# Optimization experiments

Measured on AMD Instinct MI355X. Metric: run time of the kernel, lower is better.

## Reference

```python
import jax, jax.numpy as jnp
import numpy as np
import math

B, S, D, H = 2, 2048, 2048, 16
DH = D // H
SCALE = math.sqrt(DH)


def setup_inputs() -> dict:
    key = jax.random.key(0)
    ks = jax.random.split(key, 9)
    x = jax.random.normal(ks[0], (B, S, D), dtype=jnp.float32)
    # causal mask: True above the diagonal -> masked (matches masked_fill(mask, -inf))
    mask = jnp.triu(jnp.ones((S, S), dtype=jnp.bool_), k=1)
    std = 0.02
    wq = jax.random.normal(ks[1], (D, D), jnp.float32) * std
    wk = jax.random.normal(ks[2], (D, D), jnp.float32) * std
    wv = jax.random.normal(ks[3], (D, D), jnp.float32) * std
    wo = jax.random.normal(ks[4], (D, D), jnp.float32) * std
    bq = jnp.zeros((D,), jnp.float32)
    bk = jnp.zeros((D,), jnp.float32)
    bv = jnp.zeros((D,), jnp.float32)
    bo = jnp.zeros((D,), jnp.float32)
    return {"x": x, "mask": mask, "wq": wq, "bq": bq, "wk": wk, "bk": bk,
            "wv": wv, "bv": bv, "wo": wo, "bo": bo}


def reference(x, mask, wq, bq, wk, bk, wv, bv, wo, bo):
    b, s, d = x.shape
    # projections (nn.Linear: y = x @ W^T + b)
    q = (x @ wq.T + bq).reshape(b, s, H, DH).transpose(0, 2, 1, 3)  # [b,h,s,dh]
    k = (x @ wk.T + bk).reshape(b, s, H, DH).transpose(0, 2, 1, 3)
    v = (x @ wv.T + bv).reshape(b, s, H, DH).transpose(0, 2, 1, 3)
    scores = jnp.einsum('bhqd,bhkd->bhqk', q, k) / SCALE
    scores = jnp.where(mask[None, None, :, :], -jnp.inf, scores)
    attn = jax.nn.softmax(scores, axis=-1)
    out = jnp.einsum('bhqk,bhkd->bhqd', attn, v)  # [b,h,s,dh]
    out = out.transpose(0, 2, 1, 3).reshape(b, s, d)
    return out @ wo.T + bo
```

## Files before the change

kernel.cpp:

```cpp
#include <hip/hip_runtime.h>
#include <hip/hip_bf16.h>


using u16 = unsigned short;
typedef float  f32x4  __attribute__((ext_vector_type(4)));
typedef short  short8 __attribute__((ext_vector_type(8)));

#define DEV __device__ __forceinline__

constexpr int Bc = 2, Sc = 2048, Dc = 2048, Hc = 16, DHc = 128, Mc = 4096, Kc = 2048;
constexpr float RSCALE = 0.08838834764831845f;
constexpr float L2E    = 1.44269504088896341f;

DEV u16 f2bf(float f) { __bf16 h = (__bf16)f; return __builtin_bit_cast(u16, h); }

DEV void gload_lds16(const void* gsrc, void* lds) {
  __builtin_amdgcn_global_load_lds(
      (const __attribute__((address_space(1))) unsigned int*)gsrc,
      (__attribute__((address_space(3))) unsigned int*)lds, 16, 0, 0);
}

__global__ void cast_all(const float* __restrict__ x, const float* __restrict__ wq,
                         const float* __restrict__ wk, const float* __restrict__ wv,
                         const float* __restrict__ wo, u16* __restrict__ XB,
                         u16* __restrict__ WQKV, u16* __restrict__ WOb) {
  const int i = blockIdx.x * blockDim.x + threadIdx.x;
  const float4* src;
  u16* dst;
  if (i < 2097152)      { src = (const float4*)x  + i;             dst = XB   + (size_t)i * 4; }
  else if (i < 3145728) { src = (const float4*)wq + (i - 2097152); dst = WQKV + (size_t)(i - 2097152) * 4; }
  else if (i < 4194304) { src = (const float4*)wk + (i - 3145728); dst = WQKV + 4194304 + (size_t)(i - 3145728) * 4; }
  else if (i < 5242880) { src = (const float4*)wv + (i - 4194304); dst = WQKV + 8388608 + (size_t)(i - 4194304) * 4; }
  else                  { src = (const float4*)wo + (i - 5242880); dst = WOb  + (size_t)(i - 5242880) * 4; }
  float4 v = *src;
  u16 o0 = f2bf(v.x), o1 = f2bf(v.y), o2 = f2bf(v.z), o3 = f2bf(v.w);
  dst[0] = o0; dst[1] = o1; dst[2] = o2; dst[3] = o3;
}

__global__ __launch_bounds__(512, 2) void gemm8p_qkv(
    const u16* __restrict__ A, const u16* __restrict__ W,
    const float* __restrict__ bq, const float* __restrict__ bk,
    const float* __restrict__ bv,
    u16* __restrict__ q_out, u16* __restrict__ k_out, u16* __restrict__ v_out) {
  __shared__ u16 lsA[2][256 * 64];
  __shared__ u16 lsB[2][256 * 64];
  const int tid = threadIdx.x;
  const int lane = tid & 63;
  const int w = tid >> 6;
  const int wr = w >> 2, wc = w & 3;
  const int l15 = lane & 15, l4 = lane >> 4;

  const int id = blockIdx.x;
  const int wg = (id & 7) * 48 + (id >> 3);
  const int bx = wg >> 4;
  const int by = wg & 15;
  const int m0 = by * 256, n0 = bx * 256;

  constexpr int NT = Kc / 64;

  const int srow = tid >> 3;
  const int spc = tid & 7;
  const int slc = spc ^ (srow & 7);

  auto stA = [&](int buf, int t, int mq, int h) {
    const int r = h * 128 + mq * 64 + srow;
    gload_lds16(A + (size_t)(m0 + r) * Kc + t * 64 + slc * 8,
                &lsA[buf][(h * 128 + mq * 64) * 64 + tid * 8]);
  };
  auto stB = [&](int buf, int t, int nq, int j) {
    const int rr = j * 64 + srow;
    const int n = nq * 32 + (rr >> 5) * 64 + (rr & 31);
    gload_lds16(W + (size_t)(n0 + n) * Kc + t * 64 + slc * 8,
                &lsB[buf][(nq * 128 + j * 64) * 64 + tid * 8]);
  };

  const int pc0 = l4 ^ (l15 & 7);
  const int pc1 = (4 + l4) ^ (l15 & 7);
  const int rA = wr * 128 + l15;
  const int rB = wc * 32 + l15;

  f32x4 acc[8][4] = {};
  short8 af[8], b0[4], b1[4];

  auto ldA = [&](int buf, int mq) {
#pragma unroll
    for (int fm = 0; fm < 4; ++fm) {
      const u16* base = &lsA[buf][(rA + mq * 64 + fm * 16) * 64];
      af[fm * 2 + 0] = *(const short8*)(base + pc0 * 8);
      af[fm * 2 + 1] = *(const short8*)(base + pc1 * 8);
    }
  };
  auto ldB = [&](int buf, int nq, short8* bf) {
#pragma unroll
    for (int fr = 0; fr < 2; ++fr) {
      const u16* base = &lsB[buf][(nq * 128 + rB + fr * 16) * 64];
      bf[fr * 2 + 0] = *(const short8*)(base + pc0 * 8);
      bf[fr * 2 + 1] = *(const short8*)(base + pc1 * 8);
    }
  };
  auto mma = [&](const short8* bf, int mo, int no) {
#pragma unroll
    for (int ks = 0; ks < 2; ++ks)
#pragma unroll
      for (int fm = 0; fm < 4; ++fm)
#pragma unroll
        for (int fr = 0; fr < 2; ++fr)
          acc[mo + fm][no + fr] = __builtin_amdgcn_mfma_f32_16x16x32_bf16(
              af[fm * 2 + ks], bf[fr * 2 + ks], acc[mo + fm][no + fr], 0, 0, 0);
  };

  stA(0, 0, 0, 0); stA(0, 0, 0, 1); stA(0, 0, 1, 0); stA(0, 0, 1, 1);
  stB(0, 0, 0, 0); stB(0, 0, 0, 1); stB(0, 0, 1, 0); stB(0, 0, 1, 1);
  stA(1, 1, 0, 0); stA(1, 1, 0, 1); stB(1, 1, 0, 0); stB(1, 1, 0, 1);
  asm volatile("s_waitcnt vmcnt(4)" ::: "memory");
  __builtin_amdgcn_s_barrier();

#pragma unroll 1
  for (int u = 0; u < NT; ++u) {
    const int c = u & 1;
    ldA(c, 0); ldB(c, 0, b0);
    if (u + 1 < NT) { stA(c ^ 1, u + 1, 1, 0); stA(c ^ 1, u + 1, 1, 1); }
    __builtin_amdgcn_s_barrier();
    asm volatile("s_waitcnt lgkmcnt(0)" ::: "memory");
    __builtin_amdgcn_s_setprio(1); mma(b0, 0, 0); __builtin_amdgcn_s_setprio(0);
    __builtin_amdgcn_s_barrier();
    ldB(c, 1, b1);
    if (u + 1 < NT) { stB(c ^ 1, u + 1, 1, 0); stB(c ^ 1, u + 1, 1, 1); }
    __builtin_amdgcn_s_barrier();
    asm volatile("s_waitcnt lgkmcnt(0)" ::: "memory");
    __builtin_amdgcn_s_setprio(1); mma(b1, 0, 2); __builtin_amdgcn_s_setprio(0);
    __builtin_amdgcn_s_barrier();
    ldA(c, 1);
    if (u + 2 < NT) { stA(c, u + 2, 0, 0); stA(c, u + 2, 0, 1); }
    __builtin_amdgcn_s_barrier();
    asm volatile("s_waitcnt lgkmcnt(0)" ::: "memory");
    __builtin_amdgcn_s_setprio(1); mma(b0, 4, 0); __builtin_amdgcn_s_setprio(0);
    __builtin_amdgcn_s_barrier();
    if (u + 2 < NT) { stB(c, u + 2, 0, 0); stB(c, u + 2, 0, 1); }
    __builtin_amdgcn_s_barrier();
    __builtin_amdgcn_s_setprio(1); mma(b1, 4, 2); __builtin_amdgcn_s_setprio(0);
    if (u + 2 < NT)      asm volatile("s_waitcnt vmcnt(4)" ::: "memory");
    else if (u + 1 < NT) asm volatile("s_waitcnt vmcnt(0)" ::: "memory");
    __builtin_amdgcn_s_barrier();
  }

  const int sec = n0 >> 11;
  const int n0s = n0 & 2047;
  const float* bias = sec == 0 ? bq : (sec == 1 ? bk : bv);
  u16* dst = sec == 0 ? q_out : (sec == 1 ? k_out : v_out);
  const float scl = sec == 0 ? RSCALE : 1.0f;
#pragma unroll
  for (int fg = 0; fg < 4; ++fg) {
    const int n2 = n0s + wc * 64 + fg * 16 + l15;
    const float bv_ = bias[n2];
    const int h = n2 >> 7, dh = n2 & 127;
#pragma unroll
    for (int fmg = 0; fmg < 8; ++fmg)
#pragma unroll
      for (int r = 0; r < 4; ++r) {
        const int m = m0 + wr * 128 + fmg * 16 + l4 * 4 + r;
        const int bb = m >> 11, s = m & 2047;
        dst[((size_t)(bb * Hc + h) * Sc + s) * DHc + dh] = f2bf((acc[fmg][fg][r] + bv_) * scl);
      }
  }
}

__global__ __launch_bounds__(256) void gemm_bt_out(
    const u16* __restrict__ A, const u16* __restrict__ W,
    const float* __restrict__ bias0, float* __restrict__ f_out) {
  __shared__ u16 lsA[2][128 * 32];
  __shared__ u16 lsB[2][128 * 32];
  const int tid = threadIdx.x;
  const int lane = tid & 63;
  const int w = tid >> 6;
  const int wr = w >> 1, wc = w & 1;
  const int l15 = lane & 15, l4 = lane >> 4;
  const int m0 = blockIdx.y * 128;
  const int n0 = blockIdx.x * 128;

  f32x4 acc[4][4] = {};

  auto stage = [&](int buf, int t) {
    const int k0 = t * 32;
#pragma unroll
    for (int c = 0; c < 2; ++c) {
      int p = c * 256 + tid;
      int row = p >> 2;
      int lg = (p & 3) ^ (row & 3);
      gload_lds16(A + (size_t)(m0 + row) * Kc + k0 + lg * 8, &lsA[buf][p * 8]);
    }
#pragma unroll
    for (int c = 0; c < 2; ++c) {
      int p = c * 256 + tid;
      int row = p >> 2;
      int lg = (p & 3) ^ (row & 3);
      gload_lds16(W + (size_t)(n0 + row) * Kc + k0 + lg * 8, &lsB[buf][p * 8]);
    }
  };

  auto compute = [&](int buf) {
    short8 af[4], bf[4];
#pragma unroll
    for (int mf = 0; mf < 4; ++mf) {
      int row = wr * 64 + mf * 16 + l15;
      int pc = l4 ^ (row & 3);
      af[mf] = *(const short8*)&lsA[buf][row * 32 + pc * 8];
    }
#pragma unroll
    for (int nf = 0; nf < 4; ++nf) {
      int row = wc * 64 + nf * 16 + l15;
      int pc = l4 ^ (row & 3);
      bf[nf] = *(const short8*)&lsB[buf][row * 32 + pc * 8];
    }
#pragma unroll
    for (int mf = 0; mf < 4; ++mf)
#pragma unroll
      for (int nf = 0; nf < 4; ++nf)
        acc[mf][nf] = __builtin_amdgcn_mfma_f32_16x16x32_bf16(af[mf], bf[nf], acc[mf][nf], 0, 0, 0);
  };

  stage(0, 0);
  __syncthreads();
  int buf = 0;
  const int NT = Kc / 32;
  for (int t = 0; t < NT - 1; ++t) {
    stage(buf ^ 1, t + 1);
    compute(buf);
    __syncthreads();
    buf ^= 1;
  }
  compute(buf);

#pragma unroll
  for (int nf = 0; nf < 4; ++nf) {
    const int n = n0 + wc * 64 + nf * 16 + l15;
    const float bias = bias0[n];
#pragma unroll
    for (int mf = 0; mf < 4; ++mf)
#pragma unroll
      for (int r = 0; r < 4; ++r) {
        const int m = m0 + wr * 64 + mf * 16 + l4 * 4 + r;
        f_out[(size_t)m * Dc + n] = acc[mf][nf][r] + bias;
      }
  }
}

__global__ void transpose_v(const u16* __restrict__ V, u16* __restrict__ VT) {
  __shared__ u16 t[32][33];
  const int bh = blockIdx.z;
  const int s0 = blockIdx.x * 32;
  const int d0 = blockIdx.y * 32;
  const int tx = threadIdx.x, ty = threadIdx.y;
#pragma unroll
  for (int k = 0; k < 4; ++k)
    t[ty + 8 * k][tx] = V[((size_t)bh * Sc + s0 + ty + 8 * k) * DHc + d0 + tx];
  __syncthreads();
#pragma unroll
  for (int k = 0; k < 4; ++k)
    VT[((size_t)bh * DHc + d0 + ty + 8 * k) * Sc + s0 + tx] = t[tx][ty + 8 * k];
}

__global__ __launch_bounds__(256) void fattn(
    const u16* __restrict__ Qb, const u16* __restrict__ Kb,
    const u16* __restrict__ VTb, u16* __restrict__ AO) {
  __shared__ u16 lsK[2][64 * 128];
  __shared__ u16 lsV[2][128 * 64];
  __shared__ u16 lsP[4][16 * 64];

  const int tid = threadIdx.x;
  const int lane = tid & 63;
  const int w = tid >> 6;
  const int l15 = lane & 15, l4 = lane >> 4;

  const int id = blockIdx.x;
  const int xcd = id & 7, seq = id >> 3;
  const int bh = xcd + 8 * (seq >> 4);
  const int pair = seq & 15;

  const int b = bh >> 4, h = bh & 15;
  const size_t kbase = (size_t)bh * Sc * DHc;
  const size_t vbase = (size_t)bh * DHc * Sc;

#pragma unroll 1
  for (int qsel = 0; qsel < 2; ++qsel) {
    const int qt = qsel ? (31 - pair) : pair;
    const int q0 = qt * 64;
    const int ntiles = qt + 1;

    const size_t qbase = ((size_t)bh * Sc + q0 + w * 16 + l15) * DHc;
    short8 qf[4];
#pragma unroll
    for (int ks = 0; ks < 4; ++ks)
      qf[ks] = *(const short8*)&Qb[qbase + ks * 32 + l4 * 8];

    float m_run[4], l_run[4];
#pragma unroll
    for (int r = 0; r < 4; ++r) { m_run[r] = -__builtin_inff(); l_run[r] = 0.f; }
    f32x4 o_acc[8] = {};

    auto stageKV = [&](int sb, int ti) {
      const int kv0 = ti * 64;
#pragma unroll
      for (int c = 0; c < 4; ++c) {
        int p = c * 256 + tid;
        int row = p >> 4, ph = p & 15;
        int lg = (ph & 8) | ((ph ^ row) & 7);
        gload_lds16(Kb + kbase + (size_t)(kv0 + row) * DHc + lg * 8, &lsK[sb][p * 8]);
      }
#pragma unroll
      for (int c = 0; c < 4; ++c) {
        int p = c * 256 + tid;
        int row = p >> 3, ph = p & 7;
        int lg = ph ^ (row & 7);
        gload_lds16(VTb + vbase + (size_t)row * Sc + kv0 + lg * 8, &lsV[sb][p * 8]);
      }
    };

    stageKV(0, 0);
    asm volatile("s_waitcnt vmcnt(0)" ::: "memory");
    __syncthreads();

    int buf = 0;
#pragma unroll 1
    for (int ti = 0; ti < ntiles; ++ti) {
      const int kv0 = ti * 64;
      if (ti + 1 < ntiles) stageKV(buf ^ 1, ti + 1);

      f32x4 s[4] = {};
      __builtin_amdgcn_s_setprio(1);
#pragma unroll
      for (int nf = 0; nf < 4; ++nf) {
        int row = nf * 16 + l15;
#pragma unroll
        for (int ks = 0; ks < 4; ++ks) {
          int lg = ks * 4 + l4;
          int pc = (lg & 8) | ((lg ^ row) & 7);
          short8 kf = *(const short8*)&lsK[buf][row * 128 + pc * 8];
          s[nf] = __builtin_amdgcn_mfma_f32_16x16x32_bf16(qf[ks], kf, s[nf], 0, 0, 0);
        }
      }
      __builtin_amdgcn_s_setprio(0);

      if (kv0 == q0) {
#pragma unroll
        for (int nf = 0; nf < 4; ++nf) {
          int kc = nf * 16 + l15;
#pragma unroll
          for (int r = 0; r < 4; ++r)
            if (kc > w * 16 + l4 * 4 + r) s[nf][r] = -__builtin_inff();
        }
      }
      float alpha[4];
#pragma unroll
      for (int r = 0; r < 4; ++r) {
        float mx = fmaxf(fmaxf(s[0][r], s[1][r]), fmaxf(s[2][r], s[3][r]));
        mx = fmaxf(mx, __shfl_xor(mx, 1));
        mx = fmaxf(mx, __shfl_xor(mx, 2));
        mx = fmaxf(mx, __shfl_xor(mx, 4));
        mx = fmaxf(mx, __shfl_xor(mx, 8));
        float mnew = fmaxf(m_run[r], mx);
        alpha[r] = __builtin_amdgcn_exp2f((m_run[r] - mnew) * L2E);
        m_run[r] = mnew;
      }
#pragma unroll
      for (int nf = 0; nf < 4; ++nf)
#pragma unroll
        for (int r = 0; r < 4; ++r)
          s[nf][r] = __builtin_amdgcn_exp2f((s[nf][r] - m_run[r]) * L2E);
#pragma unroll
      for (int r = 0; r < 4; ++r) {
        float sm = s[0][r] + s[1][r] + s[2][r] + s[3][r];
        sm += __shfl_xor(sm, 1);
        sm += __shfl_xor(sm, 2);
        sm += __shfl_xor(sm, 4);
        sm += __shfl_xor(sm, 8);
        l_run[r] = l_run[r] * alpha[r] + sm;
      }
#pragma unroll
      for (int nf2 = 0; nf2 < 8; ++nf2)
#pragma unroll
        for (int r = 0; r < 4; ++r) o_acc[nf2][r] *= alpha[r];

#pragma unroll
      for (int nf = 0; nf < 4; ++nf)
#pragma unroll
        for (int r = 0; r < 4; ++r) {
          int rif = l4 * 4 + r;
          int kc = nf * 16 + l15;
          int pc = (kc >> 3) ^ (rif & 7);
          lsP[w][rif * 64 + pc * 8 + (kc & 7)] = f2bf(s[nf][r]);
        }
      asm volatile("s_waitcnt lgkmcnt(0)" ::: "memory");

      __builtin_amdgcn_s_setprio(1);
#pragma unroll
      for (int ks = 0; ks < 2; ++ks) {
        int pc = (ks * 4 + l4) ^ (l15 & 7);
        short8 pa = *(const short8*)&lsP[w][l15 * 64 + pc * 8];
#pragma unroll
        for (int nf2 = 0; nf2 < 8; ++nf2) {
          int vrow = nf2 * 16 + l15;
          int vpc = (ks * 4 + l4) ^ (vrow & 7);
          short8 vb = *(const short8*)&lsV[buf][vrow * 64 + vpc * 8];
          o_acc[nf2] = __builtin_amdgcn_mfma_f32_16x16x32_bf16(pa, vb, o_acc[nf2], 0, 0, 0);
        }
      }
      __builtin_amdgcn_s_setprio(0);

      asm volatile("s_waitcnt vmcnt(0)" ::: "memory");
      __syncthreads();
      buf ^= 1;
    }

#pragma unroll
    for (int nf2 = 0; nf2 < 8; ++nf2)
#pragma unroll
      for (int r = 0; r < 4; ++r) {
        int qr = q0 + w * 16 + l4 * 4 + r;
        float ov = o_acc[nf2][r] / l_run[r];
        AO[((size_t)(b * Sc + qr)) * Dc + h * DHc + nf2 * 16 + l15] = f2bf(ov);
      }
    __syncthreads();
  }
}

extern "C" void kernel_launch(void* const* d_in, const int* in_sizes, int n_in,
                              void* d_out, int out_size, void* d_ws, size_t ws_size,
                              hipStream_t stream) {
  const float* x  = (const float*)d_in[0];
  const float* wq = (const float*)d_in[2];
  const float* bq = (const float*)d_in[3];
  const float* wk = (const float*)d_in[4];
  const float* bk = (const float*)d_in[5];
  const float* wv = (const float*)d_in[6];
  const float* bv = (const float*)d_in[7];
  const float* wo = (const float*)d_in[8];
  const float* bo = (const float*)d_in[9];
  float* out = (float*)d_out;

  char* ws = (char*)d_ws;
  u16* WQKV = (u16*)(ws + 0);
  u16* WOb  = (u16*)(ws + 25165824);
  u16* XB   = (u16*)(ws + 33554432);
  u16* Qb   = (u16*)(ws + 50331648);
  u16* Kb   = (u16*)(ws + 67108864);
  u16* Vb   = (u16*)(ws + 83886080);
  u16* VTb  = (u16*)(ws + 100663296);
  u16* AO   = XB;

  cast_all<<<dim3(24576), dim3(256), 0, stream>>>(x, wq, wk, wv, wo, XB, WQKV, WOb);
  gemm8p_qkv<<<dim3(384), dim3(512), 0, stream>>>(XB, WQKV, bq, bk, bv, Qb, Kb, Vb);
  transpose_v<<<dim3(64, 4, 32), dim3(32, 8), 0, stream>>>(Vb, VTb);
  fattn<<<dim3(512), dim3(256), 0, stream>>>(Qb, Kb, VTb, AO);
  gemm_bt_out<<<dim3(16, 32), dim3(256), 0, stream>>>(AO, WOb, bo, out);
}
```

Measured before the change: 445.7 us.

## Unify QKV and output projections into templated 8-wave pipelined GEMM

Replaces the 256x256 QKV GEMM and the simple 128x128 output GEMM with a single templated 512-thread, double-buffered GEMM using a two-phase pipeline and XOR-swizzled LDS. QKV now uses 128x256 tiles with 768 blocks, and the output projection uses 256x128 tiles with 256 blocks and K-step 64 in place of the old 4-wave kernel. The aim is better CU occupancy and wave balance for QKV and a faster, better-pipelined output projection. The cost is less data reuse per QKV tile and hand-tuned vmcnt immediates that must match the load counts exactly.

New measurement: 425.5 us. 1.05x faster.

```diff
diff --git a/kernel.cpp b/kernel.cpp
--- a/kernel.cpp
+++ b/kernel.cpp
@@ -37,211 +37,165 @@
   dst[0] = o0; dst[1] = o1; dst[2] = o2; dst[3] = o3;
 }
 
-__global__ __launch_bounds__(512, 2) void gemm8p_qkv(
+template <int BM, int BN, int WM, int WN, int EPI>
+__global__ __launch_bounds__(512, 2) void gemm2p(
     const u16* __restrict__ A, const u16* __restrict__ W,
-    const float* __restrict__ bq, const float* __restrict__ bk,
-    const float* __restrict__ bv,
-    u16* __restrict__ q_out, u16* __restrict__ k_out, u16* __restrict__ v_out) {
-  __shared__ u16 lsA[2][256 * 64];
-  __shared__ u16 lsB[2][256 * 64];
+    const float* __restrict__ bias0, const float* __restrict__ bias1,
+    const float* __restrict__ bias2,
+    u16* __restrict__ q_out, u16* __restrict__ k_out, u16* __restrict__ v_out,
+    float* __restrict__ f_out) {
+  constexpr int LA  = BM / 64;
+  constexpr int LBH = BN / 128;
+  constexpr int NH  = BN / 2;
+  static_assert(LA + 2 * LBH == 6, "vmcnt immediates assume 6");
+  constexpr int NWR = (EPI == 0) ? 6144 : 2048;
+  constexpr int NBX = NWR / BN, NBY = Mc / BM, TOT = NBX * NBY, PX = TOT / 8;
+  constexpr int NT = Kc / 64;
+
+  __shared__ u16 lsA[2][BM * 64];
+  __shared__ u16 lsB[2][BN * 64];
+
   const int tid = threadIdx.x;
   const int lane = tid & 63;
   const int w = tid >> 6;
-  const int wr = w >> 2, wc = w & 3;
+  const int wr = w / WN, wc = w % WN;
   const int l15 = lane & 15, l4 = lane >> 4;
 
   const int id = blockIdx.x;
-  const int wg = (id & 7) * 48 + (id >> 3);
-  const int bx = wg >> 4;
-  const int by = wg & 15;
-  const int m0 = by * 256, n0 = bx * 256;
-
-  constexpr int NT = Kc / 64;
+  const int wg = (id & 7) * PX + (id >> 3);
+  const int bx = wg / NBY, by = wg % NBY;
+  const int m0 = by * BM, n0 = bx * BN;
 
   const int srow = tid >> 3;
   const int spc = tid & 7;
   const int slc = spc ^ (srow & 7);
 
-  auto stA = [&](int buf, int t, int mq, int h) {
-    const int r = h * 128 + mq * 64 + srow;
-    gload_lds16(A + (size_t)(m0 + r) * Kc + t * 64 + slc * 8,
-                &lsA[buf][(h * 128 + mq * 64) * 64 + tid * 8]);
+  auto stA = [&](int buf, int t, int j) {
+    gload_lds16(A + (size_t)(m0 + j * 64 + srow) * Kc + t * 64 + slc * 8,
+                &lsA[buf][j * 4096 + tid * 8]);
   };
   auto stB = [&](int buf, int t, int nq, int j) {
-    const int rr = j * 64 + srow;
-    const int n = nq * 32 + (rr >> 5) * 64 + (rr & 31);
+    const int wp = j * 64 + srow;
+    const int n = (wp >> 5) * 64 + nq * 32 + (wp & 31);
     gload_lds16(W + (size_t)(n0 + n) * Kc + t * 64 + slc * 8,
-                &lsB[buf][(nq * 128 + j * 64) * 64 + tid * 8]);
+                &lsB[buf][(nq * NH + j * 64) * 64 + tid * 8]);
   };
 
   const int pc0 = l4 ^ (l15 & 7);
   const int pc1 = (4 + l4) ^ (l15 & 7);
-  const int rA = wr * 128 + l15;
-  const int rB = wc * 32 + l15;
-
-  f32x4 acc[8][4] = {};
+
+  f32x4 acc[4][4] = {};
   short8 af[8], b0[4], b1[4];
 
-  auto ldA = [&](int buf, int mq) {
+  auto ldA = [&](int buf) {
 #pragma unroll
     for (int fm = 0; fm < 4; ++fm) {
-      const u16* base = &lsA[buf][(rA + mq * 64 + fm * 16) * 64];
+      const u16* base = &lsA[buf][(wr * 64 + fm * 16 + l15) * 64];
       af[fm * 2 + 0] = *(const short8*)(base + pc0 * 8);
       af[fm * 2 + 1] = *(const short8*)(base + pc1 * 8);
     }
   };
   auto ldB = [&](int buf, int nq, short8* bf) {
 #pragma unroll
-    for (int fr = 0; fr < 2; ++fr) {
-      const u16* base = &lsB[buf][(nq * 128 + rB + fr * 16) * 64];
-      bf[fr * 2 + 0] = *(const short8*)(base + pc0 * 8);
-      bf[fr * 2 + 1] = *(const short8*)(base + pc1 * 8);
+    for (int f = 0; f < 2; ++f) {
+      const u16* base = &lsB[buf][(nq * NH + wc * 32 + f * 16 + l15) * 64];
+      bf[f * 2 + 0] = *(const short8*)(base + pc0 * 8);
+      bf[f * 2 + 1] = *(const short8*)(base + pc1 * 8);
     }
   };
-  auto mma = [&](const short8* bf, int mo, int no) {
+  auto mma = [&](const short8* bf, int nq) {
 #pragma unroll
     for (int ks = 0; ks < 2; ++ks)
 #pragma unroll
       for (int fm = 0; fm < 4; ++fm)
 #pragma unroll
-        for (int fr = 0; fr < 2; ++fr)
-          acc[mo + fm][no + fr] = __builtin_amdgcn_mfma_f32_16x16x32_bf16(
-              af[fm * 2 + ks], bf[fr * 2 + ks], acc[mo + fm][no + fr], 0, 0, 0);
+        for (int f = 0; f < 2; ++f)
+          acc[fm][nq * 2 + f] = __builtin_amdgcn_mfma_f32_16x16x32_bf16(
+              af[fm * 2 + ks], bf[f * 2 + ks], acc[fm][nq * 2 + f], 0, 0, 0);
   };
 
-  stA(0, 0, 0, 0); stA(0, 0, 0, 1); stA(0, 0, 1, 0); stA(0, 0, 1, 1);
-  stB(0, 0, 0, 0); stB(0, 0, 0, 1); stB(0, 0, 1, 0); stB(0, 0, 1, 1);
-  stA(1, 1, 0, 0); stA(1, 1, 0, 1); stB(1, 1, 0, 0); stB(1, 1, 0, 1);
-  asm volatile("s_waitcnt vmcnt(4)" ::: "memory");
+#pragma unroll
+  for (int j = 0; j < LA; ++j) stA(0, 0, j);
+#pragma unroll
+  for (int j = 0; j < LBH; ++j) stB(0, 0, 0, j);
+#pragma unroll
+  for (int j = 0; j < LBH; ++j) stB(0, 0, 1, j);
+#pragma unroll
+  for (int j = 0; j < LA; ++j) stA(1, 1, j);
+#pragma unroll
+  for (int j = 0; j < LBH; ++j) stB(1, 1, 0, j);
+  if constexpr (LA + LBH == 4) asm volatile("s_waitcnt vmcnt(4)" ::: "memory");
+  else                         asm volatile("s_waitcnt vmcnt(5)" ::: "memory");
   __builtin_amdgcn_s_barrier();
 
 #pragma unroll 1
   for (int u = 0; u < NT; ++u) {
     const int c = u & 1;
-    ldA(c, 0); ldB(c, 0, b0);
-    if (u + 1 < NT) { stA(c ^ 1, u + 1, 1, 0); stA(c ^ 1, u + 1, 1, 1); }
+    ldA(c);
+    ldB(c, 0, b0);
+    if (u + 1 < NT) {
+#pragma unroll
+      for (int j = 0; j < LBH; ++j) stB(c ^ 1, u + 1, 1, j);
+    }
     __builtin_amdgcn_s_barrier();
     asm volatile("s_waitcnt lgkmcnt(0)" ::: "memory");
-    __builtin_amdgcn_s_setprio(1); mma(b0, 0, 0); __builtin_amdgcn_s_setprio(0);
+    __builtin_amdgcn_s_setprio(1); mma(b0, 0); __builtin_amdgcn_s_setprio(0);
+    if (u + 1 < NT) asm volatile("s_waitcnt vmcnt(6)" ::: "memory");
+    else            asm volatile("s_waitcnt vmcnt(0)" ::: "memory");
     __builtin_amdgcn_s_barrier();
     ldB(c, 1, b1);
-    if (u + 1 < NT) { stB(c ^ 1, u + 1, 1, 0); stB(c ^ 1, u + 1, 1, 1); }
+    if (u + 2 < NT) {
+#pragma unroll
+      for (int j = 0; j < LA; ++j) stA(c, u + 2, j);
+#pragma unroll
+      for (int j = 0; j < LBH; ++j) stB(c, u + 2, 0, j);
+    }
     __builtin_amdgcn_s_barrier();
     asm volatile("s_waitcnt lgkmcnt(0)" ::: "memory");
-    __builtin_amdgcn_s_setprio(1); mma(b1, 0, 2); __builtin_amdgcn_s_setprio(0);
-    __builtin_amdgcn_s_barrier();
-    ldA(c, 1);
-    if (u + 2 < NT) { stA(c, u + 2, 0, 0); stA(c, u + 2, 0, 1); }
-    __builtin_amdgcn_s_barrier();
-    asm volatile("s_waitcnt lgkmcnt(0)" ::: "memory");
-    __builtin_amdgcn_s_setprio(1); mma(b0, 4, 0); __builtin_amdgcn_s_setprio(0);
-    __builtin_amdgcn_s_barrier();
-    if (u + 2 < NT) { stB(c, u + 2, 0, 0); stB(c, u + 2, 0, 1); }
-    __builtin_amdgcn_s_barrier();
-    __builtin_amdgcn_s_setprio(1); mma(b1, 4, 2); __builtin_amdgcn_s_setprio(0);
-    if (u + 2 < NT)      asm volatile("s_waitcnt vmcnt(4)" ::: "memory");
-    else if (u + 1 < NT) asm volatile("s_waitcnt vmcnt(0)" ::: "memory");
+    __builtin_amdgcn_s_setprio(1); mma(b1, 1); __builtin_amdgcn_s_setprio(0);
+    if (u + 2 < NT) {
+      asm volatile("s_waitcnt vmcnt(6)" ::: "memory");
+    } else if (u + 1 < NT) {
+      if constexpr (LBH == 2) asm volatile("s_waitcnt vmcnt(2)" ::: "memory");
+      else                    asm volatile("s_waitcnt vmcnt(1)" ::: "memory");
+    }
     __builtin_amdgcn_s_barrier();
   }
 
-  const int sec = n0 >> 11;
-  const int n0s = n0 & 2047;
-  const float* bias = sec == 0 ? bq : (sec == 1 ? bk : bv);
-  u16* dst = sec == 0 ? q_out : (sec == 1 ? k_out : v_out);
-  const float scl = sec == 0 ? RSCALE : 1.0f;
-#pragma unroll
-  for (int fg = 0; fg < 4; ++fg) {
-    const int n2 = n0s + wc * 64 + fg * 16 + l15;
-    const float bv_ = bias[n2];
-    const int h = n2 >> 7, dh = n2 & 127;
-#pragma unroll
-    for (int fmg = 0; fmg < 8; ++fmg)
-#pragma unroll
-      for (int r = 0; r < 4; ++r) {
-        const int m = m0 + wr * 128 + fmg * 16 + l4 * 4 + r;
-        const int bb = m >> 11, s = m & 2047;
-        dst[((size_t)(bb * Hc + h) * Sc + s) * DHc + dh] = f2bf((acc[fmg][fg][r] + bv_) * scl);
-      }
-  }
-}
-
-__global__ __launch_bounds__(256) void gemm_bt_out(
-    const u16* __restrict__ A, const u16* __restrict__ W,
-    const float* __restrict__ bias0, float* __restrict__ f_out) {
-  __shared__ u16 lsA[2][128 * 32];
-  __shared__ u16 lsB[2][128 * 32];
-  const int tid = threadIdx.x;
-  const int lane = tid & 63;
-  const int w = tid >> 6;
-  const int wr = w >> 1, wc = w & 1;
-  const int l15 = lane & 15, l4 = lane >> 4;
-  const int m0 = blockIdx.y * 128;
-  const int n0 = blockIdx.x * 128;
-
-  f32x4 acc[4][4] = {};
-
-  auto stage = [&](int buf, int t) {
-    const int k0 = t * 32;
-#pragma unroll
-    for (int c = 0; c < 2; ++c) {
-      int p = c * 256 + tid;
-      int row = p >> 2;
-      int lg = (p & 3) ^ (row & 3);
-      gload_lds16(A + (size_t)(m0 + row) * Kc + k0 + lg * 8, &lsA[buf][p * 8]);
-    }
-#pragma unroll
-    for (int c = 0; c < 2; ++c) {
-      int p = c * 256 + tid;
-      int row = p >> 2;
-      int lg = (p & 3) ^ (row & 3);
-      gload_lds16(W + (size_t)(n0 + row) * Kc + k0 + lg * 8, &lsB[buf][p * 8]);
-    }
-  };
-
-  auto compute = [&](int buf) {
-    short8 af[4], bf[4];
-#pragma unroll
-    for (int mf = 0; mf < 4; ++mf) {
-      int row = wr * 64 + mf * 16 + l15;
-      int pc = l4 ^ (row & 3);
-      af[mf] = *(const short8*)&lsA[buf][row * 32 + pc * 8];
-    }
+  if constexpr (EPI == 0) {
+    const int sec = n0 >> 11;
+    const int n0s = n0 & 2047;
+    const float* bias = sec == 0 ? bias0 : (sec == 1 ? bias1 : bias2);
+    u16* dst = sec == 0 ? q_out : (sec == 1 ? k_out : v_out);
+    const float scl = sec == 0 ? RSCALE : 1.0f;
 #pragma unroll
     for (int nf = 0; nf < 4; ++nf) {
-      int row = wc * 64 + nf * 16 + l15;
-      int pc = l4 ^ (row & 3);
-      bf[nf] = *(const short8*)&lsB[buf][row * 32 + pc * 8];
-    }
-#pragma unroll
-    for (int mf = 0; mf < 4; ++mf)
-#pragma unroll
-      for (int nf = 0; nf < 4; ++nf)
-        acc[mf][nf] = __builtin_amdgcn_mfma_f32_16x16x32_bf16(af[mf], bf[nf], acc[mf][nf], 0, 0, 0);
-  };
-
-  stage(0, 0);
-  __syncthreads();
-  int buf = 0;
-  const int NT = Kc / 32;
-  for (int t = 0; t < NT - 1; ++t) {
-    stage(buf ^ 1, t + 1);
-    compute(buf);
-    __syncthreads();
-    buf ^= 1;
-  }
-  compute(buf);
-
-#pragma unroll
-  for (int nf = 0; nf < 4; ++nf) {
-    const int n = n0 + wc * 64 + nf * 16 + l15;
-    const float bias = bias0[n];
-#pragma unroll
-    for (int mf = 0; mf < 4; ++mf)
-#pragma unroll
-      for (int r = 0; r < 4; ++r) {
-        const int m = m0 + wr * 64 + mf * 16 + l4 * 4 + r;
-        f_out[(size_t)m * Dc + n] = acc[mf][nf][r] + bias;
-      }
+      const int n2 = n0s + wc * 64 + nf * 16 + l15;
+      const float bv_ = bias[n2];
+      const int h = n2 >> 7, dh = n2 & 127;
+#pragma unroll
+      for (int fm = 0; fm < 4; ++fm)
+#pragma unroll
+        for (int r = 0; r < 4; ++r) {
+          const int m = m0 + wr * 64 + fm * 16 + l4 * 4 + r;
+          const int bb = m >> 11, s = m & 2047;
+          dst[((size_t)(bb * Hc + h) * Sc + s) * DHc + dh] =
+              f2bf((acc[fm][nf][r] + bv_) * scl);
+        }
+    }
+  } else {
+#pragma unroll
+    for (int nf = 0; nf < 4; ++nf) {
+      const int n = n0 + wc * 64 + nf * 16 + l15;
+      const float bv_ = bias0[n];
+#pragma unroll
+      for (int fm = 0; fm < 4; ++fm)
+#pragma unroll
+        for (int r = 0; r < 4; ++r) {
+          const int m = m0 + wr * 64 + fm * 16 + l4 * 4 + r;
+          f_out[(size_t)m * Dc + n] = acc[fm][nf][r] + bv_;
+        }
+    }
   }
 }
 
@@ -449,8 +403,10 @@
   u16* AO   = XB;
 
   cast_all<<<dim3(24576), dim3(256), 0, stream>>>(x, wq, wk, wv, wo, XB, WQKV, WOb);
-  gemm8p_qkv<<<dim3(384), dim3(512), 0, stream>>>(XB, WQKV, bq, bk, bv, Qb, Kb, Vb);
+  gemm2p<128, 256, 2, 4, 0><<<dim3(768), dim3(512), 0, stream>>>(
+      XB, WQKV, bq, bk, bv, Qb, Kb, Vb, nullptr);
   transpose_v<<<dim3(64, 4, 32), dim3(32, 8), 0, stream>>>(Vb, VTb);
   fattn<<<dim3(512), dim3(256), 0, stream>>>(Qb, Kb, VTb, AO);
-  gemm_bt_out<<<dim3(16, 32), dim3(256), 0, stream>>>(AO, WOb, bo, out);
-}
+  gemm2p<256, 128, 4, 2, 1><<<dim3(256), dim3(512), 0, stream>>>(
+      AO, WOb, bo, nullptr, nullptr, nullptr, nullptr, nullptr, out);
+}
```
